# Optimization experiments

Hardware: AMD Instinct MI355X
Metric: run time of the kernel (lower is better)

## Reference

```python
import jax, jax.numpy as jnp
import numpy as np

NUM_ROUNDS = 2
NUM_REVERSE_ROUNDS = 2


def _scatter_mean(x, src, dst, n):
    # PyG mean aggregation: out[i] = mean_{(src->i) in E} x[src]; 0 if no in-edges.
    deg = jax.ops.segment_sum(jnp.ones((src.shape[0],), x.dtype), dst, num_segments=n)
    s = jax.ops.segment_sum(x[src], dst, num_segments=n)
    return s / jnp.maximum(deg, 1.0)[:, None]


def setup_inputs() -> dict:
    key = jax.random.key(0)
    ks = jax.random.split(key, 12)
    N_TEXT, N_NON, E, EMB, R = 100000, 10000, 500000, 256, 500
    N = N_TEXT + N_NON
    PRED_IN = 4 * EMB + 2 * 2 + 2 * 2 * (NUM_ROUNDS + NUM_REVERSE_ROUNDS)  # 1044
    return {
        "h_id_tensor": jax.random.randint(ks[0], (E,), 0, N),
        "r_id_tensor": jax.random.randint(ks[1], (E,), 0, R),
        "t_id_tensor": jax.random.randint(ks[2], (E,), 0, N),
        "q_emb": jax.random.normal(ks[3], (EMB,), jnp.float32),
        "entity_embs": jax.random.normal(ks[4], (N_TEXT, EMB), jnp.float32),
        "num_non_text_entities": N_NON,
        "relation_embs": jax.random.normal(ks[5], (R, EMB), jnp.float32),
        "topic_entity_one_hot": jax.random.uniform(ks[6], (N, 2), jnp.float32),
        "non_text_emb": jax.random.normal(ks[7], (1, EMB), jnp.float32),
        "W1": jax.random.normal(ks[8], (PRED_IN, EMB), jnp.float32) * 0.02,
        "b1": jnp.zeros((EMB,), jnp.float32),
        "W2": jax.random.normal(ks[9], (EMB, 1), jnp.float32) * 0.02,
        "b2": jnp.zeros((1,), jnp.float32),
    }


def reference(h_id_tensor, r_id_tensor, t_id_tensor, q_emb, entity_embs,
              num_non_text_entities, relation_embs, topic_entity_one_hot,
              non_text_emb, W1, b1, W2, b2):
    n = entity_embs.shape[0] + num_non_text_entities
    # h_e base: text entity embs + broadcast non-text embedding
    h_e0 = jnp.concatenate(
        [entity_embs, jnp.broadcast_to(non_text_emb, (num_non_text_entities, non_text_emb.shape[1]))],
        axis=0)
    h_e_list = [h_e0, topic_entity_one_hot]
    # DDE forward rounds: messages flow h_id -> t_id
    h_pe = topic_entity_one_hot
    for _ in range(NUM_ROUNDS):
        h_pe = _scatter_mean(h_pe, h_id_tensor, t_id_tensor, n)
        h_e_list.append(h_pe)
    # reverse rounds: messages flow t_id -> h_id
    h_pe = topic_entity_one_hot
    for _ in range(NUM_REVERSE_ROUNDS):
        h_pe = _scatter_mean(h_pe, t_id_tensor, h_id_tensor, n)
        h_e_list.append(h_pe)
    h_e = jnp.concatenate(h_e_list, axis=1)  # [N, emb + 2 + 2*(R+Rr)]
    e = h_id_tensor.shape[0]
    h_triple = jnp.concatenate(
        [jnp.broadcast_to(q_emb[None, :], (e, q_emb.shape[0])),
         h_e[h_id_tensor],
         relation_embs[r_id_tensor],
         h_e[t_id_tensor]], axis=1)  # [E, 1044]
    hidden = jax.nn.relu(h_triple @ W1 + b1)
    return hidden @ W2 + b2
```

## Files before the change

### kernel.cpp

```cpp
#include <hip/hip_runtime.h>
#include <stdint.h>

#define EMB 256
#define LDK 288
#define DDE 10

typedef __attribute__((ext_vector_type(8))) short short8;
typedef __attribute__((ext_vector_type(4))) float f32x4;

__device__ __forceinline__ unsigned short f2bf(float f) {
    union { float f; unsigned int u; } v; v.f = f;
    unsigned int u = v.u;
    unsigned int r = (u + 0x7FFFu + ((u >> 16) & 1u)) >> 16;
    return (unsigned short)r;
}
__device__ __forceinline__ float bf2f(unsigned short b) {
    union { unsigned int u; float f; } v; v.u = ((unsigned int)b) << 16;
    return v.f;
}

#define FPSCALE 1048576.0f
#define FPINV   (1.0f / 1048576.0f)

__device__ __forceinline__ unsigned long long pack2(float a, float b) {
    unsigned int ua = (unsigned int)(a * FPSCALE);
    unsigned int ub = (unsigned int)(b * FPSCALE);
    return ((unsigned long long)ua << 36) | ((unsigned long long)ub << 10);
}


__global__ void k_scatter_r1(const int* __restrict__ h_id, const int* __restrict__ t_id,
                             const float2* __restrict__ topic,
                             unsigned long long* __restrict__ fwd,
                             unsigned long long* __restrict__ rev, int E) {
    int e = blockIdx.x * blockDim.x + threadIdx.x;
    if (e >= E) return;
    int h = h_id[e], t = t_id[e];
    float2 th = topic[h];
    float2 tt = topic[t];
    atomicAdd(&fwd[t], pack2(th.x, th.y) | 1ULL);
    atomicAdd(&rev[h], pack2(tt.x, tt.y) | 1ULL);
}

__global__ void k_norm1(const unsigned long long* __restrict__ fwd,
                        const unsigned long long* __restrict__ rev,
                        float2* __restrict__ d1n, float2* __restrict__ r1n, int N) {
    int n = blockIdx.x * blockDim.x + threadIdx.x;
    if (n >= N) return;
    unsigned long long f = fwd[n], r = rev[n];
    float df = fmaxf((float)(f & 0x3FFULL), 1.0f);
    float dr = fmaxf((float)(r & 0x3FFULL), 1.0f);
    d1n[n] = make_float2((float)((f >> 36) & 0x3FFFFFFULL) * FPINV / df,
                         (float)((f >> 10) & 0x3FFFFFFULL) * FPINV / df);
    r1n[n] = make_float2((float)((r >> 36) & 0x3FFFFFFULL) * FPINV / dr,
                         (float)((r >> 10) & 0x3FFFFFFULL) * FPINV / dr);
}

__global__ void k_scatter_r2(const int* __restrict__ h_id, const int* __restrict__ t_id,
                             const float2* __restrict__ d1n, const float2* __restrict__ r1n,
                             unsigned long long* __restrict__ s2,
                             unsigned long long* __restrict__ sr2, int E) {
    int e = blockIdx.x * blockDim.x + threadIdx.x;
    if (e >= E) return;
    int h = h_id[e], t = t_id[e];
    float2 dh = d1n[h];
    float2 rt = r1n[t];
    atomicAdd(&s2[t], pack2(dh.x, dh.y));
    atomicAdd(&sr2[h], pack2(rt.x, rt.y));
}

__global__ void k_norm2(const unsigned long long* __restrict__ fwd,
                        const unsigned long long* __restrict__ rev,
                        const unsigned long long* __restrict__ s2,
                        const unsigned long long* __restrict__ sr2,
                        float2* __restrict__ d2n, float2* __restrict__ r2n, int N) {
    int n = blockIdx.x * blockDim.x + threadIdx.x;
    if (n >= N) return;
    float df = fmaxf((float)(fwd[n] & 0x3FFULL), 1.0f);
    float dr = fmaxf((float)(rev[n] & 0x3FFULL), 1.0f);
    unsigned long long a = s2[n], b = sr2[n];
    d2n[n] = make_float2((float)((a >> 36) & 0x3FFFFFFULL) * FPINV / df,
                         (float)((a >> 10) & 0x3FFFFFFULL) * FPINV / df);
    r2n[n] = make_float2((float)((b >> 36) & 0x3FFFFFFULL) * FPINV / dr,
                         (float)((b >> 10) & 0x3FFFFFFULL) * FPINV / dr);
}


__global__ void k_build_he(const float4* __restrict__ entity, const float4* __restrict__ nontext,
                           const float2* __restrict__ topic,
                           const float2* __restrict__ d1, const float2* __restrict__ d2,
                           const float2* __restrict__ r1, const float2* __restrict__ r2,
                           ushort4* __restrict__ he, int n_text, int N, int Mpad) {
    int idx = blockIdx.x * blockDim.x + threadIdx.x;
    int total = Mpad * (LDK / 4);
    if (idx >= total) return;
    int n = idx / (LDK / 4);
    int q = idx - n * (LDK / 4);
    float4 v = make_float4(0.f, 0.f, 0.f, 0.f);
    if (n < N) {
        if (q < 64) {
            v = (n < n_text) ? entity[n * 64 + q] : nontext[q];
        } else if (q == 64) {
            float2 a = topic[n], b = d1[n];
            v = make_float4(a.x, a.y, b.x, b.y);
        } else if (q == 65) {
            float2 a = d2[n], b = r1[n];
            v = make_float4(a.x, a.y, b.x, b.y);
        } else if (q == 66) {
            float2 a = r2[n];
            v = make_float4(a.x, a.y, 0.f, 0.f);
        }
    }
    he[idx] = make_ushort4(f2bf(v.x), f2bf(v.y), f2bf(v.z), f2bf(v.w));
}

__global__ void k_build_wT(const float* __restrict__ W1, unsigned short* __restrict__ wT) {
    int idx = blockIdx.x * blockDim.x + threadIdx.x;
    if (idx >= 512 * LDK) return;
    int j = idx / LDK;
    int k = idx - j * LDK;
    int col   = (j < EMB) ? j : (j - EMB);
    int baseE = (j < EMB) ? 256 : 778;
    int baseD = (j < EMB) ? 512 : 1034;
    float v = 0.0f;
    if (k < EMB)            v = W1[(long long)(baseE + k) * EMB + col];
    else if (k < EMB + DDE) v = W1[(long long)(baseD + (k - EMB)) * EMB + col];
    wT[idx] = f2bf(v);
}

__global__ void k_build_pr(const float* __restrict__ q, const float* __restrict__ rel,
                           const float* __restrict__ W1, const float* __restrict__ b1,
                           float* __restrict__ Pr) {
    int r = blockIdx.x;
    int j = threadIdx.x;
    float acc = b1[j];
    for (int k = 0; k < EMB; ++k)
        acc = fmaf(q[k], W1[(long long)k * EMB + j], acc);
    const float* relr = rel + (long long)r * EMB;
    for (int k = 0; k < EMB; ++k)
        acc = fmaf(relr[k], W1[(long long)(522 + k) * EMB + j], acc);
    Pr[(long long)r * EMB + j] = acc;
}

__global__ __launch_bounds__(256) void k_gemm(const unsigned short* __restrict__ he,
                                              const unsigned short* __restrict__ wT,
                                              unsigned short* __restrict__ Ph,
                                              unsigned short* __restrict__ Pt,
                                              int Mpad) {
    __shared__ __align__(16) unsigned short lA[128 * 32];
    __shared__ __align__(16) unsigned short lB[128 * 32];
    const int t = threadIdx.x;
    const int lane = t & 63;
    const int w = t >> 6;
    const int br = blockIdx.x >> 2;
    const int bc = blockIdx.x & 3;
    const int wr = w >> 1;
    const int wc = w & 1;

    f32x4 acc[4][4];
#pragma unroll
    for (int r = 0; r < 4; ++r)
#pragma unroll
        for (int c = 0; c < 4; ++c)
            acc[r][c] = (f32x4){0.f, 0.f, 0.f, 0.f};

    const char* baseA = (const char*)he + (size_t)(br * 128) * (LDK * 2);
    const char* baseB = (const char*)wT + (size_t)(bc * 128) * (LDK * 2);

    for (int k0 = 0; k0 < LDK; k0 += 32) {
        __syncthreads();
#pragma unroll
        for (int i = 0; i < 2; ++i) {
            const int off  = (i * 256 + t) * 16;
            const int row  = off >> 6;
            const int colb = off & 63;
            const char* srcA = baseA + (size_t)row * (LDK * 2) + k0 * 2 + colb;
            const char* srcB = baseB + (size_t)row * (LDK * 2) + k0 * 2 + colb;
            char* dA = (char*)lA + i * 4096 + w * 1024;
            char* dB = (char*)lB + i * 4096 + w * 1024;
            __builtin_amdgcn_global_load_lds((const __attribute__((address_space(1))) void*)srcA,
                                             (__attribute__((address_space(3))) void*)dA, 16, 0, 0);
            __builtin_amdgcn_global_load_lds((const __attribute__((address_space(1))) void*)srcB,
                                             (__attribute__((address_space(3))) void*)dB, 16, 0, 0);
        }
        __syncthreads();

        short8 af[4], bfr[4];
#pragma unroll
        for (int r = 0; r < 4; ++r) {
            int arow = wr * 64 + r * 16 + (lane & 15);
            af[r] = *(const short8*)(lA + arow * 32 + (lane >> 4) * 8);
        }
#pragma unroll
        for (int c = 0; c < 4; ++c) {
            int brow = wc * 64 + c * 16 + (lane & 15);
            bfr[c] = *(const short8*)(lB + brow * 32 + (lane >> 4) * 8);
        }
#pragma unroll
        for (int r = 0; r < 4; ++r)
#pragma unroll
            for (int c = 0; c < 4; ++c)
                acc[r][c] = __builtin_amdgcn_mfma_f32_16x16x32_bf16(af[r], bfr[c], acc[r][c], 0, 0, 0);
    }

    unsigned short* Pout = (bc < 2) ? Ph : Pt;
    const int nbase = ((bc & 1) * 128) + wc * 64;
    const int mbase = br * 128 + wr * 64 + (lane >> 4) * 4;
#pragma unroll
    for (int r = 0; r < 4; ++r) {
#pragma unroll
        for (int c = 0; c < 4; ++c) {
            int n = nbase + c * 16 + (lane & 15);
#pragma unroll
            for (int i = 0; i < 4; ++i) {
                int m = mbase + r * 16 + i;
                Pout[(size_t)m * EMB + n] = f2bf(acc[r][c][i]);
            }
        }
    }
}

__global__ __launch_bounds__(256) void k_edge(
    const int* __restrict__ h_id, const int* __restrict__ r_id, const int* __restrict__ t_id,
    const unsigned short* __restrict__ Ph, const unsigned short* __restrict__ Pt,
    const float* __restrict__ Pr, const float* __restrict__ W2, const float* __restrict__ b2,
    float* __restrict__ out, int E) {
    int lane = threadIdx.x & 63;
    int gw = (blockIdx.x * blockDim.x + threadIdx.x) >> 6;
    int nw = (gridDim.x * blockDim.x) >> 6;
    float4 w2 = *(const float4*)(W2 + 4 * lane);
    float bb = b2[0];
    for (int e = gw; e < E; e += nw) {
        int h = h_id[e], r = r_id[e], t = t_id[e];
        ushort4 ph = *(const ushort4*)(Ph + (long long)h * EMB + 4 * lane);
        ushort4 pt = *(const ushort4*)(Pt + (long long)t * EMB + 4 * lane);
        float4 pr = *(const float4*)(Pr + (long long)r * EMB + 4 * lane);
        float v, acc;
        v = pr.x + bf2f(ph.x) + bf2f(pt.x); acc  = fmaxf(v, 0.f) * w2.x;
        v = pr.y + bf2f(ph.y) + bf2f(pt.y); acc += fmaxf(v, 0.f) * w2.y;
        v = pr.z + bf2f(ph.z) + bf2f(pt.z); acc += fmaxf(v, 0.f) * w2.z;
        v = pr.w + bf2f(ph.w) + bf2f(pt.w); acc += fmaxf(v, 0.f) * w2.w;
#pragma unroll
        for (int m = 32; m >= 1; m >>= 1) acc += __shfl_xor(acc, m, 64);
        if (lane == 0) out[e] = acc + bb;
    }
}


extern "C" void kernel_launch(void* const* d_in, const int* in_sizes, int n_in,
                              void* d_out, int out_size, void* d_ws, size_t ws_size,
                              hipStream_t stream) {
    const int*   h_id    = (const int*)d_in[0];
    const int*   r_id    = (const int*)d_in[1];
    const int*   t_id    = (const int*)d_in[2];
    const float* q       = (const float*)d_in[3];
    const float* entity  = (const float*)d_in[4];
    const float* rel     = (const float*)d_in[6];
    const float* topic   = (const float*)d_in[7];
    const float* nontext = (const float*)d_in[8];
    const float* W1      = (const float*)d_in[9];
    const float* b1      = (const float*)d_in[10];
    const float* W2      = (const float*)d_in[11];
    const float* b2      = (const float*)d_in[12];

    const int E      = in_sizes[0];
    const int n_text = in_sizes[4] / EMB;
    const int N      = in_sizes[7] / 2;
    const int R      = in_sizes[6] / EMB;
    const int Mpad   = (N + 127) & ~127;

    char* p = (char*)d_ws;
    auto alloc = [&](size_t bytes) {
        char* r = p;
        p += (bytes + 255) & ~(size_t)255;
        return r;
    };
    unsigned long long* fwd = (unsigned long long*)alloc((size_t)Mpad * 8);
    unsigned long long* rev = (unsigned long long*)alloc((size_t)Mpad * 8);
    unsigned long long* s2  = (unsigned long long*)alloc((size_t)Mpad * 8);
    unsigned long long* sr2 = (unsigned long long*)alloc((size_t)Mpad * 8);
    size_t zero_bytes = (size_t)(p - (char*)d_ws);
    float2* d1n = (float2*)alloc((size_t)Mpad * 8);
    float2* r1n = (float2*)alloc((size_t)Mpad * 8);
    float2* d2n = (float2*)alloc((size_t)Mpad * 8);
    float2* r2n = (float2*)alloc((size_t)Mpad * 8);
    unsigned short* he = (unsigned short*)alloc((size_t)Mpad * LDK * 2);
    unsigned short* wT = (unsigned short*)alloc((size_t)512 * LDK * 2);
    float*          Pr = (float*)alloc((size_t)R * EMB * 4);
    unsigned short* Ph = (unsigned short*)alloc((size_t)Mpad * EMB * 2);
    unsigned short* Pt = (unsigned short*)alloc((size_t)Mpad * EMB * 2);

    hipMemsetAsync(d_ws, 0, zero_bytes, stream);

    const int T = 256;
    k_scatter_r1<<<(E + T - 1) / T, T, 0, stream>>>(h_id, t_id, (const float2*)topic, fwd, rev, E);
    k_norm1<<<(Mpad + T - 1) / T, T, 0, stream>>>(fwd, rev, d1n, r1n, Mpad);
    k_scatter_r2<<<(E + T - 1) / T, T, 0, stream>>>(h_id, t_id, d1n, r1n, s2, sr2, E);
    k_norm2<<<(Mpad + T - 1) / T, T, 0, stream>>>(fwd, rev, s2, sr2, d2n, r2n, Mpad);

    int totQ = Mpad * (LDK / 4);
    k_build_he<<<(totQ + T - 1) / T, T, 0, stream>>>(
        (const float4*)entity, (const float4*)nontext, (const float2*)topic,
        d1n, d2n, r1n, r2n, (ushort4*)he, n_text, N, Mpad);
    k_build_wT<<<(512 * LDK + T - 1) / T, T, 0, stream>>>(W1, wT);
    k_build_pr<<<R, EMB, 0, stream>>>(q, rel, W1, b1, Pr);

    k_gemm<<<(Mpad / 128) * 4, T, 0, stream>>>(he, wT, Ph, Pt, Mpad);

    k_edge<<<4096, T, 0, stream>>>(h_id, r_id, t_id, Ph, Pt, Pr, W2, b2, (float*)d_out, E);
}
```

Measured before the change: 328.0 us.

## Fuse prep kernels into scatter launches, widen GEMM tile, unroll edge loop

Folds the entity-embedding bf16 copy into the first scatter launch and the W1 transpose plus relation projection into the second scatter launch, so the independent work shares blocks with the atomic-bound scatters and fewer kernels are launched. A small tail kernel now writes only the DDE columns of he. The GEMM moves to 512 threads with a 128x256 tile so each block produces a full Ph or Pt row and A tiles are loaded fewer times. The relation projection is stored in bf16 to cut gather bytes, and the edge kernel processes four edges per wave to overlap gathers. The bf16 projection adds rounding error, and the larger GEMM blocks may lower occupancy.

```diff
diff --git a/kernel.cpp b/kernel.cpp
--- a/kernel.cpp
+++ b/kernel.cpp
@@ -4,6 +4,7 @@
 #define EMB 256
 #define LDK 288
 #define DDE 10
+#define EU  4
 
 typedef __attribute__((ext_vector_type(8))) short short8;
 typedef __attribute__((ext_vector_type(4))) float f32x4;
@@ -29,17 +30,28 @@
 }
 
 
-__global__ void k_scatter_r1(const int* __restrict__ h_id, const int* __restrict__ t_id,
-                             const float2* __restrict__ topic,
-                             unsigned long long* __restrict__ fwd,
-                             unsigned long long* __restrict__ rev, int E) {
-    int e = blockIdx.x * blockDim.x + threadIdx.x;
-    if (e >= E) return;
-    int h = h_id[e], t = t_id[e];
-    float2 th = topic[h];
-    float2 tt = topic[t];
-    atomicAdd(&fwd[t], pack2(th.x, th.y) | 1ULL);
-    atomicAdd(&rev[h], pack2(tt.x, tt.y) | 1ULL);
+__global__ void k_r1_fused(const int* __restrict__ h_id, const int* __restrict__ t_id,
+                           const float2* __restrict__ topic,
+                           unsigned long long* __restrict__ fwd,
+                           unsigned long long* __restrict__ rev, int E, int SC1,
+                           const float4* __restrict__ entity, const float4* __restrict__ nontext,
+                           ushort4* __restrict__ he4, int n_text, int N) {
+    int b = blockIdx.x;
+    if (b < SC1) {
+        int e = b * 256 + threadIdx.x;
+        if (e >= E) return;
+        int h = h_id[e], t = t_id[e];
+        float2 th = topic[h];
+        float2 tt = topic[t];
+        atomicAdd(&fwd[t], pack2(th.x, th.y) | 1ULL);
+        atomicAdd(&rev[h], pack2(tt.x, tt.y) | 1ULL);
+    } else {
+        int idx = (b - SC1) * 256 + threadIdx.x;
+        int n = idx >> 6, q = idx & 63;
+        float4 v = make_float4(0.f, 0.f, 0.f, 0.f);
+        if (n < N) v = (n < n_text) ? entity[(size_t)n * 64 + q] : nontext[q];
+        he4[(size_t)n * (LDK / 4) + q] = make_ushort4(f2bf(v.x), f2bf(v.y), f2bf(v.z), f2bf(v.w));
+    }
 }
 
 __global__ void k_norm1(const unsigned long long* __restrict__ fwd,
@@ -56,17 +68,46 @@
                          (float)((r >> 10) & 0x3FFFFFFULL) * FPINV / dr);
 }
 
-__global__ void k_scatter_r2(const int* __restrict__ h_id, const int* __restrict__ t_id,
-                             const float2* __restrict__ d1n, const float2* __restrict__ r1n,
-                             unsigned long long* __restrict__ s2,
-                             unsigned long long* __restrict__ sr2, int E) {
-    int e = blockIdx.x * blockDim.x + threadIdx.x;
-    if (e >= E) return;
-    int h = h_id[e], t = t_id[e];
-    float2 dh = d1n[h];
-    float2 rt = r1n[t];
-    atomicAdd(&s2[t], pack2(dh.x, dh.y));
-    atomicAdd(&sr2[h], pack2(rt.x, rt.y));
+
+__global__ void k_r2_fused(const int* __restrict__ h_id, const int* __restrict__ t_id,
+                           const float2* __restrict__ d1n, const float2* __restrict__ r1n,
+                           unsigned long long* __restrict__ s2,
+                           unsigned long long* __restrict__ sr2, int E, int SC2, int WT_BLK,
+                           const float* __restrict__ W1,
+                           unsigned short* __restrict__ wT,
+                           const float* __restrict__ qv, const float* __restrict__ rel,
+                           const float* __restrict__ b1, unsigned short* __restrict__ Prb) {
+    int b = blockIdx.x;
+    if (b < SC2) {
+        int e = b * 256 + threadIdx.x;
+        if (e >= E) return;
+        int h = h_id[e], t = t_id[e];
+        float2 dh = d1n[h];
+        float2 rt = r1n[t];
+        atomicAdd(&s2[t], pack2(dh.x, dh.y));
+        atomicAdd(&sr2[h], pack2(rt.x, rt.y));
+    } else if (b < SC2 + WT_BLK) {
+        int idx = (b - SC2) * 256 + threadIdx.x;
+        int j = idx / LDK;
+        int k = idx - j * LDK;
+        int col   = (j < EMB) ? j : (j - EMB);
+        int baseE = (j < EMB) ? 256 : 778;
+        int baseD = (j < EMB) ? 512 : 1034;
+        float v = 0.0f;
+        if (k < EMB)            v = W1[(long long)(baseE + k) * EMB + col];
+        else if (k < EMB + DDE) v = W1[(long long)(baseD + (k - EMB)) * EMB + col];
+        wT[idx] = f2bf(v);
+    } else {
+        int r = b - SC2 - WT_BLK;
+        int j = threadIdx.x;
+        float acc = b1[j];
+        for (int k = 0; k < EMB; ++k)
+            acc = fmaf(qv[k], W1[(long long)k * EMB + j], acc);
+        const float* relr = rel + (long long)r * EMB;
+        for (int k = 0; k < EMB; ++k)
+            acc = fmaf(relr[k], W1[(long long)(522 + k) * EMB + j], acc);
+        Prb[(long long)r * EMB + j] = f2bf(acc);
+    }
 }
 
 __global__ void k_norm2(const unsigned long long* __restrict__ fwd,
@@ -85,77 +126,35 @@
                          (float)((b >> 10) & 0x3FFFFFFULL) * FPINV / dr);
 }
 
-
-__global__ void k_build_he(const float4* __restrict__ entity, const float4* __restrict__ nontext,
-                           const float2* __restrict__ topic,
-                           const float2* __restrict__ d1, const float2* __restrict__ d2,
-                           const float2* __restrict__ r1, const float2* __restrict__ r2,
-                           ushort4* __restrict__ he, int n_text, int N, int Mpad) {
+__global__ void k_he_tail(const float2* __restrict__ topic,
+                          const float2* __restrict__ d1, const float2* __restrict__ d2,
+                          const float2* __restrict__ r1, const float2* __restrict__ r2,
+                          ushort4* __restrict__ he4, int N, int Mpad) {
     int idx = blockIdx.x * blockDim.x + threadIdx.x;
-    int total = Mpad * (LDK / 4);
-    if (idx >= total) return;
-    int n = idx / (LDK / 4);
-    int q = idx - n * (LDK / 4);
+    if (idx >= Mpad * 8) return;
+    int n = idx >> 3, j = idx & 7;
     float4 v = make_float4(0.f, 0.f, 0.f, 0.f);
     if (n < N) {
-        if (q < 64) {
-            v = (n < n_text) ? entity[n * 64 + q] : nontext[q];
-        } else if (q == 64) {
-            float2 a = topic[n], b = d1[n];
-            v = make_float4(a.x, a.y, b.x, b.y);
-        } else if (q == 65) {
-            float2 a = d2[n], b = r1[n];
-            v = make_float4(a.x, a.y, b.x, b.y);
-        } else if (q == 66) {
-            float2 a = r2[n];
-            v = make_float4(a.x, a.y, 0.f, 0.f);
-        }
-    }
-    he[idx] = make_ushort4(f2bf(v.x), f2bf(v.y), f2bf(v.z), f2bf(v.w));
-}
-
-__global__ void k_build_wT(const float* __restrict__ W1, unsigned short* __restrict__ wT) {
-    int idx = blockIdx.x * blockDim.x + threadIdx.x;
-    if (idx >= 512 * LDK) return;
-    int j = idx / LDK;
-    int k = idx - j * LDK;
-    int col   = (j < EMB) ? j : (j - EMB);
-    int baseE = (j < EMB) ? 256 : 778;
-    int baseD = (j < EMB) ? 512 : 1034;
-    float v = 0.0f;
-    if (k < EMB)            v = W1[(long long)(baseE + k) * EMB + col];
-    else if (k < EMB + DDE) v = W1[(long long)(baseD + (k - EMB)) * EMB + col];
-    wT[idx] = f2bf(v);
-}
-
-__global__ void k_build_pr(const float* __restrict__ q, const float* __restrict__ rel,
-                           const float* __restrict__ W1, const float* __restrict__ b1,
-                           float* __restrict__ Pr) {
-    int r = blockIdx.x;
-    int j = threadIdx.x;
-    float acc = b1[j];
-    for (int k = 0; k < EMB; ++k)
-        acc = fmaf(q[k], W1[(long long)k * EMB + j], acc);
-    const float* relr = rel + (long long)r * EMB;
-    for (int k = 0; k < EMB; ++k)
-        acc = fmaf(relr[k], W1[(long long)(522 + k) * EMB + j], acc);
-    Pr[(long long)r * EMB + j] = acc;
-}
-
-__global__ __launch_bounds__(256) void k_gemm(const unsigned short* __restrict__ he,
+        if (j == 0)      { float2 a = topic[n], bq = d1[n]; v = make_float4(a.x, a.y, bq.x, bq.y); }
+        else if (j == 1) { float2 a = d2[n],   bq = r1[n]; v = make_float4(a.x, a.y, bq.x, bq.y); }
+        else if (j == 2) { float2 a = r2[n];               v = make_float4(a.x, a.y, 0.f, 0.f); }
+    }
+    he4[(size_t)n * (LDK / 4) + 64 + j] = make_ushort4(f2bf(v.x), f2bf(v.y), f2bf(v.z), f2bf(v.w));
+}
+
+__global__ __launch_bounds__(512) void k_gemm(const unsigned short* __restrict__ he,
                                               const unsigned short* __restrict__ wT,
                                               unsigned short* __restrict__ Ph,
-                                              unsigned short* __restrict__ Pt,
-                                              int Mpad) {
+                                              unsigned short* __restrict__ Pt) {
     __shared__ __align__(16) unsigned short lA[128 * 32];
-    __shared__ __align__(16) unsigned short lB[128 * 32];
+    __shared__ __align__(16) unsigned short lB[256 * 32];
     const int t = threadIdx.x;
     const int lane = t & 63;
     const int w = t >> 6;
-    const int br = blockIdx.x >> 2;
-    const int bc = blockIdx.x & 3;
-    const int wr = w >> 1;
-    const int wc = w & 1;
+    const int br = blockIdx.x >> 1;
+    const int bc = blockIdx.x & 1;
+    const int wr = w >> 2;
+    const int wc = w & 3;
 
     f32x4 acc[4][4];
 #pragma unroll
@@ -165,23 +164,23 @@
             acc[r][c] = (f32x4){0.f, 0.f, 0.f, 0.f};
 
     const char* baseA = (const char*)he + (size_t)(br * 128) * (LDK * 2);
-    const char* baseB = (const char*)wT + (size_t)(bc * 128) * (LDK * 2);
+    const char* baseB = (const char*)wT + (size_t)(bc * 256) * (LDK * 2);
+
+    const int rowX = t >> 2;
+    const int colb = (t & 3) * 16;
 
     for (int k0 = 0; k0 < LDK; k0 += 32) {
         __syncthreads();
-#pragma unroll
-        for (int i = 0; i < 2; ++i) {
-            const int off  = (i * 256 + t) * 16;
-            const int row  = off >> 6;
-            const int colb = off & 63;
-            const char* srcA = baseA + (size_t)row * (LDK * 2) + k0 * 2 + colb;
-            const char* srcB = baseB + (size_t)row * (LDK * 2) + k0 * 2 + colb;
-            char* dA = (char*)lA + i * 4096 + w * 1024;
-            char* dB = (char*)lB + i * 4096 + w * 1024;
+        {
+            const char* srcA  = baseA + (size_t)rowX * (LDK * 2) + k0 * 2 + colb;
+            const char* srcB0 = baseB + (size_t)rowX * (LDK * 2) + k0 * 2 + colb;
+            const char* srcB1 = baseB + (size_t)(rowX + 128) * (LDK * 2) + k0 * 2 + colb;
             __builtin_amdgcn_global_load_lds((const __attribute__((address_space(1))) void*)srcA,
-                                             (__attribute__((address_space(3))) void*)dA, 16, 0, 0);
-            __builtin_amdgcn_global_load_lds((const __attribute__((address_space(1))) void*)srcB,
-                                             (__attribute__((address_space(3))) void*)dB, 16, 0, 0);
+                                             (__attribute__((address_space(3))) void*)((char*)lA + t * 16), 16, 0, 0);
+            __builtin_amdgcn_global_load_lds((const __attribute__((address_space(1))) void*)srcB0,
+                                             (__attribute__((address_space(3))) void*)((char*)lB + t * 16), 16, 0, 0);
+            __builtin_amdgcn_global_load_lds((const __attribute__((address_space(1))) void*)srcB1,
+                                             (__attribute__((address_space(3))) void*)((char*)lB + 8192 + t * 16), 16, 0, 0);
         }
         __syncthreads();
 
@@ -203,8 +202,8 @@
                 acc[r][c] = __builtin_amdgcn_mfma_f32_16x16x32_bf16(af[r], bfr[c], acc[r][c], 0, 0, 0);
     }
 
-    unsigned short* Pout = (bc < 2) ? Ph : Pt;
-    const int nbase = ((bc & 1) * 128) + wc * 64;
+    unsigned short* Pout = bc ? Pt : Ph;
+    const int nbase = wc * 64;
     const int mbase = br * 128 + wr * 64 + (lane >> 4) * 4;
 #pragma unroll
     for (int r = 0; r < 4; ++r) {
@@ -223,26 +222,56 @@
 __global__ __launch_bounds__(256) void k_edge(
     const int* __restrict__ h_id, const int* __restrict__ r_id, const int* __restrict__ t_id,
     const unsigned short* __restrict__ Ph, const unsigned short* __restrict__ Pt,
-    const float* __restrict__ Pr, const float* __restrict__ W2, const float* __restrict__ b2,
-    float* __restrict__ out, int E) {
-    int lane = threadIdx.x & 63;
-    int gw = (blockIdx.x * blockDim.x + threadIdx.x) >> 6;
-    int nw = (gridDim.x * blockDim.x) >> 6;
+    const unsigned short* __restrict__ Prb, const float* __restrict__ W2,
+    const float* __restrict__ b2, float* __restrict__ out, int E) {
+    const int lane = threadIdx.x & 63;
+    const int gw = (blockIdx.x * blockDim.x + threadIdx.x) >> 6;
+    const int nw = (gridDim.x * blockDim.x) >> 6;
     float4 w2 = *(const float4*)(W2 + 4 * lane);
     float bb = b2[0];
-    for (int e = gw; e < E; e += nw) {
-        int h = h_id[e], r = r_id[e], t = t_id[e];
-        ushort4 ph = *(const ushort4*)(Ph + (long long)h * EMB + 4 * lane);
-        ushort4 pt = *(const ushort4*)(Pt + (long long)t * EMB + 4 * lane);
-        float4 pr = *(const float4*)(Pr + (long long)r * EMB + 4 * lane);
-        float v, acc;
-        v = pr.x + bf2f(ph.x) + bf2f(pt.x); acc  = fmaxf(v, 0.f) * w2.x;
-        v = pr.y + bf2f(ph.y) + bf2f(pt.y); acc += fmaxf(v, 0.f) * w2.y;
-        v = pr.z + bf2f(ph.z) + bf2f(pt.z); acc += fmaxf(v, 0.f) * w2.z;
-        v = pr.w + bf2f(ph.w) + bf2f(pt.w); acc += fmaxf(v, 0.f) * w2.w;
-#pragma unroll
-        for (int m = 32; m >= 1; m >>= 1) acc += __shfl_xor(acc, m, 64);
-        if (lane == 0) out[e] = acc + bb;
+    const int lo = 4 * lane;
+
+    for (int e0 = gw * EU; e0 < E; e0 += nw * EU) {
+        if (e0 + EU <= E) {
+            int h[EU], r[EU], t[EU];
+#pragma unroll
+            for (int u = 0; u < EU; ++u) {
+                h[u] = h_id[e0 + u]; r[u] = r_id[e0 + u]; t[u] = t_id[e0 + u];
+            }
+            ushort4 ph[EU], pt[EU], pr[EU];
+#pragma unroll
+            for (int u = 0; u < EU; ++u) {
+                ph[u] = *(const ushort4*)(Ph + (size_t)h[u] * EMB + lo);
+                pt[u] = *(const ushort4*)(Pt + (size_t)t[u] * EMB + lo);
+                pr[u] = *(const ushort4*)(Prb + (size_t)r[u] * EMB + lo);
+            }
+#pragma unroll
+            for (int u = 0; u < EU; ++u) {
+                float v, acc;
+                v = bf2f(pr[u].x) + bf2f(ph[u].x) + bf2f(pt[u].x); acc  = fmaxf(v, 0.f) * w2.x;
+                v = bf2f(pr[u].y) + bf2f(ph[u].y) + bf2f(pt[u].y); acc += fmaxf(v, 0.f) * w2.y;
+                v = bf2f(pr[u].z) + bf2f(ph[u].z) + bf2f(pt[u].z); acc += fmaxf(v, 0.f) * w2.z;
+                v = bf2f(pr[u].w) + bf2f(ph[u].w) + bf2f(pt[u].w); acc += fmaxf(v, 0.f) * w2.w;
+#pragma unroll
+                for (int m = 32; m >= 1; m >>= 1) acc += __shfl_xor(acc, m, 64);
+                if (lane == 0) out[e0 + u] = acc + bb;
+            }
+        } else {
+            for (int u = 0; u < E - e0; ++u) {
+                int h = h_id[e0 + u], rr = r_id[e0 + u], tt = t_id[e0 + u];
+                ushort4 ph = *(const ushort4*)(Ph + (size_t)h * EMB + lo);
+                ushort4 pt = *(const ushort4*)(Pt + (size_t)tt * EMB + lo);
+                ushort4 pr = *(const ushort4*)(Prb + (size_t)rr * EMB + lo);
+                float v, acc;
+                v = bf2f(pr.x) + bf2f(ph.x) + bf2f(pt.x); acc  = fmaxf(v, 0.f) * w2.x;
+                v = bf2f(pr.y) + bf2f(ph.y) + bf2f(pt.y); acc += fmaxf(v, 0.f) * w2.y;
+                v = bf2f(pr.z) + bf2f(ph.z) + bf2f(pt.z); acc += fmaxf(v, 0.f) * w2.z;
+                v = bf2f(pr.w) + bf2f(ph.w) + bf2f(pt.w); acc += fmaxf(v, 0.f) * w2.w;
+#pragma unroll
+                for (int m = 32; m >= 1; m >>= 1) acc += __shfl_xor(acc, m, 64);
+                if (lane == 0) out[e0 + u] = acc + bb;
+            }
+        }
     }
 }
 
@@ -284,28 +313,31 @@
     float2* r1n = (float2*)alloc((size_t)Mpad * 8);
     float2* d2n = (float2*)alloc((size_t)Mpad * 8);
     float2* r2n = (float2*)alloc((size_t)Mpad * 8);
-    unsigned short* he = (unsigned short*)alloc((size_t)Mpad * LDK * 2);
-    unsigned short* wT = (unsigned short*)alloc((size_t)512 * LDK * 2);
-    float*          Pr = (float*)alloc((size_t)R * EMB * 4);
-    unsigned short* Ph = (unsigned short*)alloc((size_t)Mpad * EMB * 2);
-    unsigned short* Pt = (unsigned short*)alloc((size_t)Mpad * EMB * 2);
+    unsigned short* he  = (unsigned short*)alloc((size_t)Mpad * LDK * 2);
+    unsigned short* wT  = (unsigned short*)alloc((size_t)512 * LDK * 2);
+    unsigned short* Prb = (unsigned short*)alloc((size_t)R * EMB * 2);
+    unsigned short* Ph  = (unsigned short*)alloc((size_t)Mpad * EMB * 2);
+    unsigned short* Pt  = (unsigned short*)alloc((size_t)Mpad * EMB * 2);
 
     hipMemsetAsync(d_ws, 0, zero_bytes, stream);
 
     const int T = 256;
-    k_scatter_r1<<<(E + T - 1) / T, T, 0, stream>>>(h_id, t_id, (const float2*)topic, fwd, rev, E);
+    const int SC1 = (E + T - 1) / T;
+    const int COPY_BLK = Mpad / 4;
+    const int SC2 = SC1;
+    const int WT_BLK = (512 * LDK) / T;
+
+    k_r1_fused<<<SC1 + COPY_BLK, T, 0, stream>>>(
+        h_id, t_id, (const float2*)topic, fwd, rev, E, SC1,
+        (const float4*)entity, (const float4*)nontext, (ushort4*)he, n_text, N);
     k_norm1<<<(Mpad + T - 1) / T, T, 0, stream>>>(fwd, rev, d1n, r1n, Mpad);
-    k_scatter_r2<<<(E + T - 1) / T, T, 0, stream>>>(h_id, t_id, d1n, r1n, s2, sr2, E);
+    k_r2_fused<<<SC2 + WT_BLK + R, T, 0, stream>>>(
+        h_id, t_id, d1n, r1n, s2, sr2, E, SC2, WT_BLK, W1, wT, q, rel, b1, Prb);
     k_norm2<<<(Mpad + T - 1) / T, T, 0, stream>>>(fwd, rev, s2, sr2, d2n, r2n, Mpad);
-
-    int totQ = Mpad * (LDK / 4);
-    k_build_he<<<(totQ + T - 1) / T, T, 0, stream>>>(
-        (const float4*)entity, (const float4*)nontext, (const float2*)topic,
-        d1n, d2n, r1n, r2n, (ushort4*)he, n_text, N, Mpad);
-    k_build_wT<<<(512 * LDK + T - 1) / T, T, 0, stream>>>(W1, wT);
-    k_build_pr<<<R, EMB, 0, stream>>>(q, rel, W1, b1, Pr);
-
-    k_gemm<<<(Mpad / 128) * 4, T, 0, stream>>>(he, wT, Ph, Pt, Mpad);
-
-    k_edge<<<4096, T, 0, stream>>>(h_id, r_id, t_id, Ph, Pt, Pr, W2, b2, (float*)d_out, E);
-}
+    k_he_tail<<<(Mpad * 8 + T - 1) / T, T, 0, stream>>>(
+        (const float2*)topic, d1n, d2n, r1n, r2n, (ushort4*)he, N, Mpad);
+
+    k_gemm<<<(Mpad / 128) * 2, 512, 0, stream>>>(he, wT, Ph, Pt);
+
+    k_edge<<<2048, T, 0, stream>>>(h_id, r_id, t_id, Ph, Pt, Prb, W2, b2, (float*)d_out, E);
+}
```

Result: faster. 305.3 us (-6.9%).
